# Optimization experiments

Measured on AMD Instinct MI355X. Metric: run time of the kernel, lower is better.

## Reference

```python
import jax, jax.numpy as jnp
import numpy as np

B, S, H = 2, 512, 1024
D = 24            # hdim_proj_dim
MLP_H = 96        # hdim_mlp_hidden
VAL_IN = 2 * H    # concat_only
OUT_HID = 2 * max(128, H // 2)  # 1024


def setup_inputs() -> dict:
    key = jax.random.key(0)
    ks = jax.random.split(key, 12)
    sc = 0.02
    return {
        "H_j": jax.random.normal(ks[0], (B, S, H), jnp.float32),
        "H_i": jax.random.normal(ks[1], (B, S, H), jnp.float32),
        "attn_mask": jnp.ones((B, S), jnp.float32),
        "p_j": jax.random.normal(ks[2], (H, D), jnp.float32) * sc,
        "p_i": jax.random.normal(ks[3], (H, D), jnp.float32) * sc,
        "W1": jax.random.normal(ks[4], (4 * D, MLP_H), jnp.float32) * sc,
        "b1": jnp.zeros((MLP_H,), jnp.float32),
        "W2": jax.random.normal(ks[5], (MLP_H, 1), jnp.float32) * sc,
        "b2": jnp.zeros((1,), jnp.float32),
        "Wv1": jax.random.normal(ks[6], (VAL_IN, OUT_HID), jnp.float32) * sc,
        "bv1": jnp.zeros((OUT_HID,), jnp.float32),
        "Wv2": jax.random.normal(ks[7], (OUT_HID, H), jnp.float32) * sc,
        "bv2": jnp.zeros((H,), jnp.float32),
        "alpha": jnp.asarray(0.05, jnp.float32),
    }


def reference(H_j, H_i, attn_mask, p_j, p_i, W1, b1, W2, b2, Wv1, bv1, Wv2, bv2, alpha):
    # Low-dim projections: [B,S,D]
    Zj = jnp.einsum('bsh,hd->bsd', H_j, p_j)
    Zi = jnp.einsum('bsh,hd->bsd', H_i, p_i)
    # 4-term pairwise features: [B,S,S,4D]
    Zj_b = jnp.broadcast_to(Zj[:, :, None, :], (B, S, S, D))
    Zi_b = jnp.broadcast_to(Zi[:, None, :, :], (B, S, S, D))
    pair = jnp.concatenate([Zj_b, Zi_b, Zj_b * Zi_b, jnp.abs(Zj_b - Zi_b)], axis=-1)
    # Pair-score MLP -> logits [B,S,S]
    h = jax.nn.relu(jnp.einsum('bjif,fm->bjim', pair, W1) + b1)
    logits = (jnp.einsum('bjim,mo->bjio', h, W2) + b2)[..., 0]
    # additive key-side mask (same as torch _expand_mask_last)
    logits = logits + (1.0 - attn_mask)[:, None, :] * jnp.finfo(logits.dtype).min
    # token_temp == 1.0 -> no scaling
    probs = jax.nn.softmax(logits, axis=-1)  # over keys i
    ctx = jnp.einsum('bji,bih->bjh', probs, H_i)  # [B,S,H]
    # Value fusion MLP (concat_only), dropout is identity in eval
    msg_in = jnp.concatenate([ctx, H_j], axis=-1)  # [B,S,2H]
    msg = jax.nn.relu(jnp.einsum('bsf,fo->bso', msg_in, Wv1) + bv1)
    msg = jnp.einsum('bso,oh->bsh', msg, Wv2) + bv2
    return alpha * msg
```

## Files before the change

kernel.cpp:

```cpp
#include <hip/hip_runtime.h>
#include <math.h>

#define B_    2
#define S_    512
#define HDIM  1024
#define D_    24
#define M_    96
#define ROWS  (B_*S_)

typedef _Float16 half8 __attribute__((ext_vector_type(8)));
typedef float    f32x4 __attribute__((ext_vector_type(4)));

__device__ __forceinline__ void transpose_tile(
    const float* __restrict__ in, _Float16* __restrict__ out,
    int R, int C, int xt, int yt, float (*tile)[33], int t) {
  int bx = xt * 32, by = yt * 32;
  int tx = t & 31, ty = t >> 5;
#pragma unroll
  for (int k = 0; k < 4; ++k)
    tile[ty + k * 8][tx] = in[(size_t)(by + ty + k * 8) * C + bx + tx];
  __syncthreads();
#pragma unroll
  for (int k = 0; k < 4; ++k)
    out[(size_t)(bx + ty + k * 8) * R + by + tx] = (_Float16)tile[tx][ty + k * 8];
}

__global__ __launch_bounds__(256) void prep_kernel(
    const float* __restrict__ Hj, const float* __restrict__ Hi,
    const float* __restrict__ pj, const float* __restrict__ pi,
    const float* __restrict__ W1, const float* __restrict__ Wv1,
    const float* __restrict__ Wv2,
    _Float16* __restrict__ HjH, _Float16* __restrict__ HiT,
    _Float16* __restrict__ Wv1T, _Float16* __restrict__ Wv2T,
    _Float16* __restrict__ Wimg, float* __restrict__ Zj,
    float* __restrict__ Zi) {
  __shared__ float tile[32][33];
  const int bid = blockIdx.x;
  const int t = threadIdx.x;

  if (bid < 4) {
    int c = bid * 256 + t;
    half8 v = {};
    if (c < 864) {
      int kc = c / 96, m = c - kc * 96;
#pragma unroll
      for (int e = 0; e < 8; ++e)
        v[e] = (_Float16)W1[(24 + kc * 8 + e) * M_ + m];
    }
    *(half8*)(Wimg + (size_t)c * 8) = v;
  } else if (bid < 1028) {
    int i = (bid - 4) * 256 + t;
    float4 v = ((const float4*)Hj)[i];
    _Float16 o[4] = {(_Float16)v.x, (_Float16)v.y, (_Float16)v.z, (_Float16)v.w};
    ((ushort4*)HjH)[i] = *(ushort4*)o;
  } else if (bid < 2052) {
    int id = bid - 1028;
    int z = id >> 9, rem = id & 511;
    transpose_tile(Hi + (size_t)z * S_ * HDIM, HiT + (size_t)z * HDIM * S_,
                   S_, HDIM, rem & 31, rem >> 5, tile, t);
  } else if (bid < 4100) {
    int id = bid - 2052;
    transpose_tile(Wv1, Wv1T, 2 * HDIM, HDIM, id & 31, id >> 5, tile, t);
  } else if (bid < 5124) {
    int id = bid - 4100;
    transpose_tile(Wv2, Wv2T, HDIM, HDIM, id & 31, id >> 5, tile, t);
  } else {
    int r = (bid - 5124) * 4 + (t >> 6);
    int lane = t & 63;
    float4 a4 = ((const float4*)(Hj + (size_t)r * HDIM))[lane];
    float4 c4 = ((const float4*)(Hi + (size_t)r * HDIM))[lane];
    float accj[D_], acci[D_];
#pragma unroll
    for (int d = 0; d < D_; ++d) { accj[d] = 0.f; acci[d] = 0.f; }
    const float* aa = (const float*)&a4;
    const float* cc = (const float*)&c4;
#pragma unroll
    for (int kk = 0; kk < 4; ++kk) {
      const float4* pj4 = (const float4*)(pj + (size_t)(lane * 4 + kk) * D_);
      const float4* pi4 = (const float4*)(pi + (size_t)(lane * 4 + kk) * D_);
      float a = aa[kk], c = cc[kk];
#pragma unroll
      for (int q = 0; q < 6; ++q) {
        float4 wj = pj4[q], wi = pi4[q];
        accj[q * 4 + 0] = fmaf(a, wj.x, accj[q * 4 + 0]);
        accj[q * 4 + 1] = fmaf(a, wj.y, accj[q * 4 + 1]);
        accj[q * 4 + 2] = fmaf(a, wj.z, accj[q * 4 + 2]);
        accj[q * 4 + 3] = fmaf(a, wj.w, accj[q * 4 + 3]);
        acci[q * 4 + 0] = fmaf(c, wi.x, acci[q * 4 + 0]);
        acci[q * 4 + 1] = fmaf(c, wi.y, acci[q * 4 + 1]);
        acci[q * 4 + 2] = fmaf(c, wi.z, acci[q * 4 + 2]);
        acci[q * 4 + 3] = fmaf(c, wi.w, acci[q * 4 + 3]);
      }
    }
#pragma unroll
    for (int d = 0; d < D_; ++d) {
      for (int off = 32; off > 0; off >>= 1) {
        accj[d] += __shfl_down(accj[d], off, 64);
        acci[d] += __shfl_down(acci[d], off, 64);
      }
    }
    if (lane == 0) {
#pragma unroll
      for (int d = 0; d < D_; ++d) {
        Zj[r * D_ + d] = accj[d];
        Zi[r * D_ + d] = acci[d];
      }
    }
  }
}

#define FOFFB   0
#define WOFFB   40960
#define ZOFFB   (WOFFB + 960*16)
#define LOGOFFB (WOFFB + 16384)
#define ZJOFFB  (LOGOFFB + 2048)
#define W2OFFB  (ZJOFFB + 96)
#define REDOFFB (W2OFFB + 384)
#define LDSB    (REDOFFB + 32)

__global__ __launch_bounds__(256) void pair_fused_kernel(
    const float* __restrict__ Zj, const float* __restrict__ Zi,
    const float* __restrict__ W1, const float* __restrict__ b1,
    const float* __restrict__ W2, const _Float16* __restrict__ Wimg,
    const float* __restrict__ mask, _Float16* __restrict__ probs) {
  __shared__ __attribute__((aligned(16))) char smem[LDSB];
  const int t = threadIdx.x;
  const int w = t >> 6, l = t & 63;
  const int lo = l & 15, hi = l >> 4;
  const int rj = blockIdx.x;
  const int b = rj >> 9;

#pragma unroll
  for (int r = 0; r < 4; ++r) {
    const _Float16* src = Wimg + (size_t)(r * 256 + w * 64 + l) * 8;
    __builtin_amdgcn_global_load_lds(
        (const __attribute__((address_space(1))) void*)src,
        (__attribute__((address_space(3))) void*)(smem + WOFFB + (r * 256 + w * 64) * 16),
        16, 0, 0);
  }
  float* zjL    = (float*)(smem + ZJOFFB);
  float* W2s    = (float*)(smem + W2OFFB);
  float* logits = (float*)(smem + LOGOFFB);
  float* red    = (float*)(smem + REDOFFB);
  if (t < D_) zjL[t] = Zj[(size_t)rj * D_ + t];
  if (t < M_) W2s[t] = W2[t];
  float aj = 0.f;
  if (t < M_) {
    aj = b1[t];
#pragma unroll
    for (int d = 0; d < D_; ++d)
      aj = fmaf(Zj[(size_t)rj * D_ + d], W1[d * M_ + t], aj);
  }
  __syncthreads();
  if (t < M_) {
    half8 v = {};
    v[0] = (_Float16)aj;
    *(half8*)(smem + WOFFB + (864 + t) * 16) = v;
  }

  half8 wf[6][3];
  float w2r[6][4];

  for (int p = 0; p < 2; ++p) {
    {
      int i = p * 256 + t;
      const float* zi = Zi + (size_t)(b * S_ + i) * D_;
      float ziv[D_];
#pragma unroll
      for (int q = 0; q < 6; ++q) {
        float4 v = ((const float4*)zi)[q];
        ziv[q * 4 + 0] = v.x; ziv[q * 4 + 1] = v.y;
        ziv[q * 4 + 2] = v.z; ziv[q * 4 + 3] = v.w;
      }
#pragma unroll
      for (int kc = 0; kc < 3; ++kc) {
        half8 v;
#pragma unroll
        for (int e = 0; e < 8; ++e) v[e] = (_Float16)ziv[kc * 8 + e];
        *(half8*)(smem + FOFFB + (kc * 256 + t) * 16) = v;
      }
#pragma unroll
      for (int kc = 0; kc < 3; ++kc) {
        half8 v;
#pragma unroll
        for (int e = 0; e < 8; ++e) {
          int d = kc * 8 + e;
          v[e] = (_Float16)(zjL[d] * ziv[d]);
        }
        *(half8*)(smem + FOFFB + ((kc + 3) * 256 + t) * 16) = v;
      }
#pragma unroll
      for (int kc = 0; kc < 3; ++kc) {
        half8 v;
#pragma unroll
        for (int e = 0; e < 8; ++e) {
          int d = kc * 8 + e;
          v[e] = (_Float16)fabsf(zjL[d] - ziv[d]);
        }
        *(half8*)(smem + FOFFB + ((kc + 6) * 256 + t) * 16) = v;
      }
      if (p == 0) {
        half8 v = {};
        v[0] = (_Float16)1.0f;
        *(half8*)(smem + FOFFB + (9 * 256 + t) * 16) = v;
      }
    }
    __syncthreads();

    if (p == 0) {
#pragma unroll
      for (int mh = 0; mh < 6; ++mh) {
#pragma unroll
        for (int ks = 0; ks < 3; ++ks) {
          int kc = ks * 4 + hi;
          int off = (kc < 10) ? (WOFFB + (kc * 96 + mh * 16 + lo) * 16) : ZOFFB;
          wf[mh][ks] = *(const half8*)(smem + off);
        }
#pragma unroll
        for (int r = 0; r < 4; ++r) w2r[mh][r] = W2s[mh * 16 + hi * 4 + r];
      }
    }

#pragma unroll
    for (int nt = 0; nt < 4; ++nt) {
      half8 ff[3];
#pragma unroll
      for (int ks = 0; ks < 3; ++ks) {
        int kc = ks * 4 + hi;
        int off = (kc < 10) ? (FOFFB + (kc * 256 + w * 64 + nt * 16 + lo) * 16) : ZOFFB;
        ff[ks] = *(const half8*)(smem + off);
      }
      f32x4 a6[6] = {};
#pragma unroll
      for (int ks = 0; ks < 3; ++ks)
#pragma unroll
        for (int mh = 0; mh < 6; ++mh)
          a6[mh] = __builtin_amdgcn_mfma_f32_16x16x32_f16(wf[mh][ks], ff[ks], a6[mh], 0, 0, 0);
      float part = 0.f;
#pragma unroll
      for (int mh = 0; mh < 6; ++mh)
#pragma unroll
        for (int r = 0; r < 4; ++r)
          part = fmaf(fmaxf(a6[mh][r], 0.f), w2r[mh][r], part);
      part += __shfl_xor(part, 16);
      part += __shfl_xor(part, 32);
      if (hi == 0) logits[p * 256 + w * 64 + nt * 16 + lo] = part;
    }
    __syncthreads();
  }

  float m1 = mask[b * S_ + t], m2 = mask[b * S_ + t + 256];
  float lg1 = logits[t]       + (1.0f - m1) * (-3.40282347e38f);
  float lg2 = logits[t + 256] + (1.0f - m2) * (-3.40282347e38f);
  float mx = fmaxf(lg1, lg2);
#pragma unroll
  for (int off = 32; off > 0; off >>= 1) mx = fmaxf(mx, __shfl_xor(mx, off));
  if (l == 0) red[w] = mx;
  __syncthreads();
  float rmax = fmaxf(fmaxf(red[0], red[1]), fmaxf(red[2], red[3]));
  float e1 = __expf(lg1 - rmax);
  float e2 = __expf(lg2 - rmax);
  float s = e1 + e2;
#pragma unroll
  for (int off = 32; off > 0; off >>= 1) s += __shfl_xor(s, off);
  if (l == 0) red[4 + w] = s;
  __syncthreads();
  float inv = 1.0f / (red[4] + red[5] + red[6] + red[7]);
  probs[(size_t)rj * S_ + t]       = (_Float16)(e1 * inv);
  probs[(size_t)rj * S_ + t + 256] = (_Float16)(e2 * inv);
}

template <bool HASA1, bool RELU, bool FINAL, bool OUTH>
__global__ __launch_bounds__(512) void mfma_gemm_kernel(
    const _Float16* __restrict__ A0, const _Float16* __restrict__ A1,
    const _Float16* __restrict__ Bt, const float* __restrict__ bias,
    const float* __restrict__ alpha_ptr, void* __restrict__ Cout,
    int M, int N, int K0, int K1,
    long aB0, long aB1, long bB, long cB) {
  __shared__ __attribute__((aligned(16))) char smem[65536];
  const int t = threadIdx.x;
  const int w = t >> 6, l = t & 63;
  const int g = w >> 2, wq = w & 3;
  const int K = K0 + K1;
  const int KH = K >> 1;
  const int NT = KH >> 5;
  const int n0 = blockIdx.x * 64, m0 = blockIdx.y * 64;
  const int zb = blockIdx.z;
  const _Float16* A0b = A0 + (size_t)zb * aB0;
  const _Float16* A1b = HASA1 ? (A1 + (size_t)zb * aB1) : nullptr;
  const _Float16* Btb = Bt + (size_t)zb * bB;
  char* gls = smem + (g << 15);

  const int sr = (wq << 4) + (l >> 2);
  const int sk = ((l & 3) ^ ((l >> 3) & 3)) << 3;

  const int mq = wq >> 1, nq = wq & 1;
  int offA[2], offB[2];
#pragma unroll
  for (int i = 0; i < 2; ++i) {
    int ra = mq * 32 + i * 16 + (l & 15);
    offA[i] = ra * 64 + (((l >> 4) ^ ((ra >> 1) & 3)) << 4);
    int rb = nq * 32 + i * 16 + (l & 15);
    offB[i] = 4096 + rb * 64 + (((l >> 4) ^ ((rb >> 1) & 3)) << 4);
  }

  f32x4 acc[2][2] = {};

  auto stage = [&](int tt) {
    char* buf = gls + (tt & 3) * 8192;
    int kg = g * KH + (tt << 5) + sk;
    const _Float16* ga;
    if (HASA1 && kg >= K0) ga = A1b + (size_t)(m0 + sr) * K1 + (kg - K0);
    else                   ga = A0b + (size_t)(m0 + sr) * K0 + kg;
    __builtin_amdgcn_global_load_lds(
        (const __attribute__((address_space(1))) void*)ga,
        (__attribute__((address_space(3))) void*)(buf + (wq << 10)), 16, 0, 0);
    const _Float16* gb = Btb + (size_t)(n0 + sr) * K + kg;
    __builtin_amdgcn_global_load_lds(
        (const __attribute__((address_space(1))) void*)gb,
        (__attribute__((address_space(3))) void*)(buf + 4096 + (wq << 10)), 16, 0, 0);
  };

  stage(0);
  stage(1);
  stage(2);

  for (int tt = 0; tt < NT; ++tt) {
    if (tt + 2 < NT)      asm volatile("s_waitcnt vmcnt(4)" ::: "memory");
    else if (tt + 1 < NT) asm volatile("s_waitcnt vmcnt(2)" ::: "memory");
    else                  asm volatile("s_waitcnt vmcnt(0)" ::: "memory");
    __builtin_amdgcn_s_barrier();
    __builtin_amdgcn_sched_barrier(0);
    const char* buf = gls + (tt & 3) * 8192;
    half8 a0 = *(const half8*)(buf + offA[0]);
    half8 a1 = *(const half8*)(buf + offA[1]);
    half8 b0 = *(const half8*)(buf + offB[0]);
    half8 b1v = *(const half8*)(buf + offB[1]);
    acc[0][0] = __builtin_amdgcn_mfma_f32_16x16x32_f16(a0, b0, acc[0][0], 0, 0, 0);
    acc[0][1] = __builtin_amdgcn_mfma_f32_16x16x32_f16(a0, b1v, acc[0][1], 0, 0, 0);
    acc[1][0] = __builtin_amdgcn_mfma_f32_16x16x32_f16(a1, b0, acc[1][0], 0, 0, 0);
    acc[1][1] = __builtin_amdgcn_mfma_f32_16x16x32_f16(a1, b1v, acc[1][1], 0, 0, 0);
    if (tt + 3 < NT) stage(tt + 3);
  }

  const int lr = l & 15, lq = l >> 4;
  float* redm = (float*)smem;
  __syncthreads();
  if (g == 1) {
#pragma unroll
    for (int mi = 0; mi < 2; ++mi)
#pragma unroll
      for (int ni = 0; ni < 2; ++ni)
#pragma unroll
        for (int rg = 0; rg < 4; ++rg)
          redm[(mq * 32 + mi * 16 + lq * 4 + rg) * 68 + nq * 32 + ni * 16 + lr] =
              acc[mi][ni][rg];
  }
  __syncthreads();
  if (g == 0) {
    const float alpha = FINAL ? *alpha_ptr : 1.0f;
    const size_t cbase = (size_t)zb * cB;
#pragma unroll
    for (int mi = 0; mi < 2; ++mi)
#pragma unroll
      for (int ni = 0; ni < 2; ++ni) {
        int col = n0 + nq * 32 + ni * 16 + lr;
        float bv = bias ? bias[col] : 0.0f;
#pragma unroll
        for (int rg = 0; rg < 4; ++rg) {
          int row = m0 + mq * 32 + mi * 16 + lq * 4 + rg;
          float x = acc[mi][ni][rg] +
                    redm[(mq * 32 + mi * 16 + lq * 4 + rg) * 68 + nq * 32 + ni * 16 + lr] +
                    bv;
          if (RELU) x = fmaxf(x, 0.f);
          if (FINAL) x *= alpha;
          if (OUTH)
            ((_Float16*)Cout)[cbase + (size_t)row * N + col] = (_Float16)x;
          else
            ((float*)Cout)[cbase + (size_t)row * N + col] = x;
        }
      }
  }
}

extern "C" void kernel_launch(void* const* d_in, const int* in_sizes, int n_in,
                              void* d_out, int out_size, void* d_ws, size_t ws_size,
                              hipStream_t stream) {
  const float* Hj   = (const float*)d_in[0];
  const float* Hi   = (const float*)d_in[1];
  const float* mask = (const float*)d_in[2];
  const float* pj   = (const float*)d_in[3];
  const float* pi   = (const float*)d_in[4];
  const float* W1   = (const float*)d_in[5];
  const float* b1   = (const float*)d_in[6];
  const float* W2   = (const float*)d_in[7];
  const float* Wv1  = (const float*)d_in[9];
  const float* bv1  = (const float*)d_in[10];
  const float* Wv2  = (const float*)d_in[11];
  const float* bv2  = (const float*)d_in[12];
  const float* alpha = (const float*)d_in[13];

  char* w = (char*)d_ws;
  float* Zj  = (float*)w;            w += (size_t)ROWS * D_ * 4;
  float* Zi  = (float*)w;            w += (size_t)ROWS * D_ * 4;
  _Float16* Wimg   = (_Float16*)w;   w += (size_t)1024 * 16;
  _Float16* probsH = (_Float16*)w;   w += (size_t)B_ * S_ * S_ * 2;
  _Float16* HjH    = (_Float16*)w;   w += (size_t)ROWS * HDIM * 2;
  _Float16* HiT    = (_Float16*)w;   w += (size_t)B_ * HDIM * S_ * 2;
  _Float16* Wv1T   = (_Float16*)w;   w += (size_t)HDIM * 2 * HDIM * 2;
  _Float16* Wv2T   = (_Float16*)w;   w += (size_t)HDIM * HDIM * 2;
  _Float16* ctxH   = (_Float16*)w;   w += (size_t)ROWS * HDIM * 2;
  _Float16* hidH   = (_Float16*)w;   w += (size_t)ROWS * HDIM * 2;
  float* out = (float*)d_out;

  prep_kernel<<<5380, 256, 0, stream>>>(Hj, Hi, pj, pi, W1, Wv1, Wv2,
                                        HjH, HiT, Wv1T, Wv2T, Wimg, Zj, Zi);

  pair_fused_kernel<<<ROWS, 256, 0, stream>>>(Zj, Zi, W1, b1, W2, Wimg,
                                              mask, probsH);

  mfma_gemm_kernel<false, false, false, true><<<dim3(16, 8, 2), 512, 0, stream>>>(
      probsH, nullptr, HiT, nullptr, nullptr, ctxH,
      S_, HDIM, S_, 0, (long)S_ * S_, 0, (long)HDIM * S_, (long)S_ * HDIM);
  mfma_gemm_kernel<true, true, false, true><<<dim3(16, 16, 1), 512, 0, stream>>>(
      ctxH, HjH, Wv1T, bv1, nullptr, hidH,
      ROWS, HDIM, HDIM, HDIM, 0, 0, 0, 0);
  mfma_gemm_kernel<false, false, true, false><<<dim3(16, 16, 1), 512, 0, stream>>>(
      hidH, nullptr, Wv2T, bv2, alpha, out,
      ROWS, HDIM, HDIM, 0, 0, 0, 0, 0);
}
```

Measured before the change: 76.22 us.

## Move projections to MFMA kernel and use 64x64 LDS-free transposes in prep

The Zj/Zi projections leave the scalar FMA plus shuffle-reduction path and move to a separate MFMA-based proj_kernel, which also writes the fp16 copy of Hj. The prep transposes now use 64x64 tiles with per-thread strided column reads and 16-byte fp16 writes instead of LDS-staged 32x32 tiles, cutting the block count. An s_setprio bump around the MFMA loop in the pair kernel is also added. The cost is an extra kernel launch, fp16 rounding of the inputs to the projection, and uncoalesced strided reads in the transposes.

```diff
diff --git a/kernel.cpp b/kernel.cpp
--- a/kernel.cpp
+++ b/kernel.cpp
@@ -10,31 +10,29 @@
 
 typedef _Float16 half8 __attribute__((ext_vector_type(8)));
 typedef float    f32x4 __attribute__((ext_vector_type(4)));
-
-__device__ __forceinline__ void transpose_tile(
+typedef unsigned short ushort8 __attribute__((ext_vector_type(8)));
+
+__device__ __forceinline__ void transpose_tile64_cache(
     const float* __restrict__ in, _Float16* __restrict__ out,
-    int R, int C, int xt, int yt, float (*tile)[33], int t) {
-  int bx = xt * 32, by = yt * 32;
-  int tx = t & 31, ty = t >> 5;
-#pragma unroll
-  for (int k = 0; k < 4; ++k)
-    tile[ty + k * 8][tx] = in[(size_t)(by + ty + k * 8) * C + bx + tx];
-  __syncthreads();
-#pragma unroll
-  for (int k = 0; k < 4; ++k)
-    out[(size_t)(bx + ty + k * 8) * R + by + tx] = (_Float16)tile[tx][ty + k * 8];
+    int R, int C, int xt, int yt, int t) {
+  int R0 = yt * 64, C0 = xt * 64;
+  int c = t >> 2, rq = (t & 3) * 16;
+  _Float16 o[16];
+  const float* src = in + (size_t)(R0 + rq) * C + C0 + c;
+#pragma unroll
+  for (int e = 0; e < 16; ++e) o[e] = (_Float16)src[(size_t)e * C];
+  _Float16* dst = out + (size_t)(C0 + c) * R + R0 + rq;
+  *(ushort8*)dst = *(ushort8*)o;
+  *(ushort8*)(dst + 8) = *(ushort8*)&o[8];
 }
 
 __global__ __launch_bounds__(256) void prep_kernel(
-    const float* __restrict__ Hj, const float* __restrict__ Hi,
-    const float* __restrict__ pj, const float* __restrict__ pi,
-    const float* __restrict__ W1, const float* __restrict__ Wv1,
-    const float* __restrict__ Wv2,
-    _Float16* __restrict__ HjH, _Float16* __restrict__ HiT,
-    _Float16* __restrict__ Wv1T, _Float16* __restrict__ Wv2T,
-    _Float16* __restrict__ Wimg, float* __restrict__ Zj,
-    float* __restrict__ Zi) {
-  __shared__ float tile[32][33];
+    const float* __restrict__ Hi, const float* __restrict__ pj,
+    const float* __restrict__ pi, const float* __restrict__ W1,
+    const float* __restrict__ Wv1, const float* __restrict__ Wv2,
+    _Float16* __restrict__ HiT, _Float16* __restrict__ Wv1T,
+    _Float16* __restrict__ Wv2T, _Float16* __restrict__ Wimg,
+    _Float16* __restrict__ PjT, _Float16* __restrict__ PiT) {
   const int bid = blockIdx.x;
   const int t = threadIdx.x;
 
@@ -48,64 +46,68 @@
         v[e] = (_Float16)W1[(24 + kc * 8 + e) * M_ + m];
     }
     *(half8*)(Wimg + (size_t)c * 8) = v;
-  } else if (bid < 1028) {
-    int i = (bid - 4) * 256 + t;
-    float4 v = ((const float4*)Hj)[i];
-    _Float16 o[4] = {(_Float16)v.x, (_Float16)v.y, (_Float16)v.z, (_Float16)v.w};
-    ((ushort4*)HjH)[i] = *(ushort4*)o;
-  } else if (bid < 2052) {
-    int id = bid - 1028;
-    int z = id >> 9, rem = id & 511;
-    transpose_tile(Hi + (size_t)z * S_ * HDIM, HiT + (size_t)z * HDIM * S_,
-                   S_, HDIM, rem & 31, rem >> 5, tile, t);
-  } else if (bid < 4100) {
-    int id = bid - 2052;
-    transpose_tile(Wv1, Wv1T, 2 * HDIM, HDIM, id & 31, id >> 5, tile, t);
-  } else if (bid < 5124) {
-    int id = bid - 4100;
-    transpose_tile(Wv2, Wv2T, HDIM, HDIM, id & 31, id >> 5, tile, t);
+  } else if (bid < 12) {
+    int id = bid - 4;
+    const float* P = (id < 4) ? pj : pi;
+    _Float16* PT = (id < 4) ? PjT : PiT;
+    int k = (id & 3) * 256 + t;
+#pragma unroll
+    for (int d = 0; d < 32; ++d) {
+      float v = (d < D_) ? P[(size_t)k * D_ + d] : 0.0f;
+      PT[(size_t)d * 1024 + k] = (_Float16)v;
+    }
+  } else if (bid < 268) {
+    int id = bid - 12;
+    int z = id >> 7, rem = id & 127;
+    transpose_tile64_cache(Hi + (size_t)z * S_ * HDIM,
+                           HiT + (size_t)z * HDIM * S_,
+                           S_, HDIM, rem & 15, rem >> 4, t);
+  } else if (bid < 780) {
+    int id = bid - 268;
+    transpose_tile64_cache(Wv1, Wv1T, 2 * HDIM, HDIM, id & 15, id >> 4, t);
   } else {
-    int r = (bid - 5124) * 4 + (t >> 6);
-    int lane = t & 63;
-    float4 a4 = ((const float4*)(Hj + (size_t)r * HDIM))[lane];
-    float4 c4 = ((const float4*)(Hi + (size_t)r * HDIM))[lane];
-    float accj[D_], acci[D_];
-#pragma unroll
-    for (int d = 0; d < D_; ++d) { accj[d] = 0.f; acci[d] = 0.f; }
-    const float* aa = (const float*)&a4;
-    const float* cc = (const float*)&c4;
-#pragma unroll
-    for (int kk = 0; kk < 4; ++kk) {
-      const float4* pj4 = (const float4*)(pj + (size_t)(lane * 4 + kk) * D_);
-      const float4* pi4 = (const float4*)(pi + (size_t)(lane * 4 + kk) * D_);
-      float a = aa[kk], c = cc[kk];
-#pragma unroll
-      for (int q = 0; q < 6; ++q) {
-        float4 wj = pj4[q], wi = pi4[q];
-        accj[q * 4 + 0] = fmaf(a, wj.x, accj[q * 4 + 0]);
-        accj[q * 4 + 1] = fmaf(a, wj.y, accj[q * 4 + 1]);
-        accj[q * 4 + 2] = fmaf(a, wj.z, accj[q * 4 + 2]);
-        accj[q * 4 + 3] = fmaf(a, wj.w, accj[q * 4 + 3]);
-        acci[q * 4 + 0] = fmaf(c, wi.x, acci[q * 4 + 0]);
-        acci[q * 4 + 1] = fmaf(c, wi.y, acci[q * 4 + 1]);
-        acci[q * 4 + 2] = fmaf(c, wi.z, acci[q * 4 + 2]);
-        acci[q * 4 + 3] = fmaf(c, wi.w, acci[q * 4 + 3]);
-      }
-    }
-#pragma unroll
-    for (int d = 0; d < D_; ++d) {
-      for (int off = 32; off > 0; off >>= 1) {
-        accj[d] += __shfl_down(accj[d], off, 64);
-        acci[d] += __shfl_down(acci[d], off, 64);
-      }
-    }
-    if (lane == 0) {
-#pragma unroll
-      for (int d = 0; d < D_; ++d) {
-        Zj[r * D_ + d] = accj[d];
-        Zi[r * D_ + d] = acci[d];
-      }
-    }
+    int id = bid - 780;
+    transpose_tile64_cache(Wv2, Wv2T, HDIM, HDIM, id & 15, id >> 4, t);
+  }
+}
+
+__global__ __launch_bounds__(64) void proj_kernel(
+    const float* __restrict__ Hj, const float* __restrict__ Hi,
+    const _Float16* __restrict__ PjT, const _Float16* __restrict__ PiT,
+    _Float16* __restrict__ HjH, float* __restrict__ Zj,
+    float* __restrict__ Zi) {
+  const int bid = blockIdx.x;
+  const int l = threadIdx.x;
+  const int lo = l & 15, hi = l >> 4;
+  const bool isj = bid < 64;
+  const int r0 = (bid & 63) * 16;
+  const float* H = isj ? Hj : Hi;
+  const _Float16* PT = isj ? PjT : PiT;
+  float* Z = isj ? Zj : Zi;
+  const float* hrow = H + (size_t)(r0 + lo) * HDIM;
+
+  f32x4 acc0 = {}, acc1 = {};
+  for (int step = 0; step < 32; ++step) {
+    const float* src = hrow + step * 32 + hi * 8;
+    float4 v0 = *(const float4*)src;
+    float4 v1 = *(const float4*)(src + 4);
+    half8 a8;
+    a8[0] = (_Float16)v0.x; a8[1] = (_Float16)v0.y;
+    a8[2] = (_Float16)v0.z; a8[3] = (_Float16)v0.w;
+    a8[4] = (_Float16)v1.x; a8[5] = (_Float16)v1.y;
+    a8[6] = (_Float16)v1.z; a8[7] = (_Float16)v1.w;
+    if (isj)
+      *(half8*)(HjH + (size_t)(r0 + lo) * HDIM + step * 32 + hi * 8) = a8;
+    half8 b0 = *(const half8*)(PT + (size_t)lo * 1024 + step * 32 + hi * 8);
+    half8 b1 = *(const half8*)(PT + (size_t)(16 + lo) * 1024 + step * 32 + hi * 8);
+    acc0 = __builtin_amdgcn_mfma_f32_16x16x32_f16(a8, b0, acc0, 0, 0, 0);
+    acc1 = __builtin_amdgcn_mfma_f32_16x16x32_f16(a8, b1, acc1, 0, 0, 0);
+  }
+#pragma unroll
+  for (int rg = 0; rg < 4; ++rg) {
+    int row = r0 + hi * 4 + rg;
+    Z[(size_t)row * D_ + lo] = acc0[rg];
+    if (lo < 8) Z[(size_t)row * D_ + 16 + lo] = acc1[rg];
   }
 }
 
@@ -231,11 +233,13 @@
         ff[ks] = *(const half8*)(smem + off);
       }
       f32x4 a6[6] = {};
+      __builtin_amdgcn_s_setprio(1);
 #pragma unroll
       for (int ks = 0; ks < 3; ++ks)
 #pragma unroll
         for (int mh = 0; mh < 6; ++mh)
           a6[mh] = __builtin_amdgcn_mfma_f32_16x16x32_f16(wf[mh][ks], ff[ks], a6[mh], 0, 0, 0);
+      __builtin_amdgcn_s_setprio(0);
       float part = 0.f;
 #pragma unroll
       for (int mh = 0; mh < 6; ++mh)
@@ -404,6 +408,8 @@
   float* Zj  = (float*)w;            w += (size_t)ROWS * D_ * 4;
   float* Zi  = (float*)w;            w += (size_t)ROWS * D_ * 4;
   _Float16* Wimg   = (_Float16*)w;   w += (size_t)1024 * 16;
+  _Float16* PjT    = (_Float16*)w;   w += (size_t)32 * 1024 * 2;
+  _Float16* PiT    = (_Float16*)w;   w += (size_t)32 * 1024 * 2;
   _Float16* probsH = (_Float16*)w;   w += (size_t)B_ * S_ * S_ * 2;
   _Float16* HjH    = (_Float16*)w;   w += (size_t)ROWS * HDIM * 2;
   _Float16* HiT    = (_Float16*)w;   w += (size_t)B_ * HDIM * S_ * 2;
@@ -413,8 +419,9 @@
   _Float16* hidH   = (_Float16*)w;   w += (size_t)ROWS * HDIM * 2;
   float* out = (float*)d_out;
 
-  prep_kernel<<<5380, 256, 0, stream>>>(Hj, Hi, pj, pi, W1, Wv1, Wv2,
-                                        HjH, HiT, Wv1T, Wv2T, Wimg, Zj, Zi);
+  prep_kernel<<<1036, 256, 0, stream>>>(Hi, pj, pi, W1, Wv1, Wv2,
+                                        HiT, Wv1T, Wv2T, Wimg, PjT, PiT);
+  proj_kernel<<<128, 64, 0, stream>>>(Hj, Hi, PjT, PiT, HjH, Zj, Zi);
 
   pair_fused_kernel<<<ROWS, 256, 0, stream>>>(Zj, Zi, W1, b1, W2, Wimg,
                                               mask, probsH);
```

New measurement: 76.07 us. About the same (-0.2%).
